# Optimization experiments

Measured on AMD Instinct MI355X. Metric: run time of the kernel, lower is better.

## Reference

```python
import jax, jax.numpy as jnp
import numpy as np

B, N, DIM = 1, 100_000, 512
HEADS, DIM_HEAD, M = 8, 64, 64


def setup_inputs() -> dict:
    key = jax.random.key(0)
    ks = jax.random.split(key, 9)
    s = 0.04  # ~ kaiming-ish scale for dim=512
    return {
        "x": jax.random.normal(ks[0], (B, N, DIM), dtype=jnp.float32),
        "temperature": jnp.full((1, HEADS, 1, 1), 0.5, dtype=jnp.float32),
        "w_slice": jax.random.normal(ks[1], (HEADS * M, DIM), dtype=jnp.float32) * s,
        "b_slice": jnp.zeros((HEADS * M,), dtype=jnp.float32),
        "w1": jax.random.normal(ks[2], (DIM_HEAD, DIM), dtype=jnp.float32) * s,
        "b1": jnp.zeros((DIM_HEAD,), dtype=jnp.float32),
        "wq": jax.random.normal(ks[3], (DIM_HEAD, DIM_HEAD), dtype=jnp.float32) * 0.125,
        "wk": jax.random.normal(ks[4], (DIM_HEAD, DIM_HEAD), dtype=jnp.float32) * 0.125,
        "wv": jax.random.normal(ks[5], (DIM_HEAD, DIM_HEAD), dtype=jnp.float32) * 0.125,
        "w3": jax.random.normal(ks[6], (DIM_HEAD, DIM_HEAD), dtype=jnp.float32) * 0.125,
        "b3": jnp.zeros((DIM_HEAD,), dtype=jnp.float32),
    }


def reference(x, temperature, w_slice, b_slice, w1, b1, wq, wk, wv, w3, b3):
    b, n, c = x.shape
    # slice logits: (B,N,H*M) -> (B,H,N,M)
    logits = jnp.einsum("bnc,ec->bne", x, w_slice) + b_slice
    logits = logits.reshape(b, n, HEADS, M).transpose(0, 2, 1, 3)
    temp = jnp.clip(temperature, 0.1, 5.0)
    w = jax.nn.softmax(logits / temp, axis=-1)          # (B,H,N,M)
    d = w.sum(axis=2)                                    # (B,H,M)
    # N -> M aggregation (w^T @ x per head)
    s_raw = jnp.einsum("bhnm,bnc->bhmc", w, x)          # (B,H,M,C)
    s = jnp.einsum("bhmc,dc->bhmd", s_raw / (d[..., None] + 1e-5), w1) + b1  # (B,H,M,dh)
    q = jnp.einsum("bhmd,ed->bhme", s, wq)
    k = jnp.einsum("bhmd,ed->bhme", s, wk)
    v = jnp.einsum("bhmd,ed->bhme", s, wv)
    scale = 1.0 / jnp.sqrt(jnp.asarray(DIM_HEAD, dtype=s.dtype))
    attn = jax.nn.softmax(jnp.einsum("bhme,bhle->bhml", q, k) * scale, axis=-1)
    s_att = jnp.einsum("bhml,bhle->bhme", attn, v)      # (B,H,M,dh)
    s_out = jnp.einsum("bhme,de->bhmd", s_att, w3) + b3
    # deslice: w @ s_out -> (B,H,N,dh) -> (B,N,H*dh)
    x_out = jnp.einsum("bhnm,bhmd->bhnd", w, s_out)
    return x_out.transpose(0, 2, 1, 3).reshape(b, n, HEADS * DIM_HEAD)
```

## Files before the change

### kernel.cpp

```cpp
#include <hip/hip_runtime.h>

typedef _Float16 f16;
typedef _Float16 f16x8 __attribute__((ext_vector_type(8)));
typedef _Float16 f16x4 __attribute__((ext_vector_type(4)));
typedef float    f32x4 __attribute__((ext_vector_type(4)));

#define N_TOK   100000
#define NPAD    100032
#define NT1     1563
#define CDIM    512
#define KSTEPS  (NPAD/32)
#define K2SPL   128

#define O_WT     ((size_t)0)
#define SZ_WT    ((size_t)512*NPAD*2)
#define O_YT     (O_WT + SZ_WT)
#define SZ_YT    ((size_t)64*NPAD*2)
#define O_WFR    (O_YT + SZ_YT)
#define SZ_WFR   ((size_t)16*4*9*64*8*2)
#define O_SPP    (O_WFR + SZ_WFR)
#define SZ_SPP   ((size_t)K2SPL*32768*4)
#define O_DPP    (O_SPP + SZ_SPP)
#define SZ_DPP   ((size_t)K2SPL*512*4)
#define O_SPRE   (O_DPP + SZ_DPP)
#define SZ_SPRE  ((size_t)32768*4)
#define O_DSTD   (O_SPRE + SZ_SPRE)
#define SZ_DSTD  ((size_t)512*4)
#define O_SOUT   (O_DSTD + SZ_DSTD)
#define SZ_SOUT  ((size_t)8*64*64*2)

__global__ void k0_pack(const float* __restrict__ wsf, const float* __restrict__ w1f,
                        f16* __restrict__ wfr) {
    int c = blockIdx.x * 256 + threadIdx.x;
    int lane = c & 63, g = c >> 6;
    int u  = g % 9,  r = g / 9;
    int we = r & 3,  kg = r >> 2;
    int col = lane & 15, quad = lane >> 4;
    int k = kg * 32 + quad * 8;
    const float* src;
    if (u < 8) src = wsf + (size_t)(we*128 + u*16 + col) * CDIM + k;
    else       src = w1f + (size_t)(we*16  + col) * CDIM + k;
    float4 a = *(const float4*)(src);
    float4 b = *(const float4*)(src + 4);
    f16x8 h;
    h[0]=(f16)a.x; h[1]=(f16)a.y; h[2]=(f16)a.z; h[3]=(f16)a.w;
    h[4]=(f16)b.x; h[5]=(f16)b.y; h[6]=(f16)b.z; h[7]=(f16)b.w;
    *(f16x8*)(wfr + (size_t)c * 8) = h;
}

#define XROW 40
#define TPITCH 72
__launch_bounds__(256, 3)
__global__ void k1_slice(const float* __restrict__ x, const float* __restrict__ temperature,
                         const f16* __restrict__ wfr, const float* __restrict__ bsl,
                         f16* __restrict__ wTf, f16* __restrict__ yTf) {
    __shared__ f16 smem[320 * TPITCH];
    f16* lX = smem;
    f16* lT = smem;
    f16* lY = smem + 256 * TPITCH;

    const int tid  = threadIdx.x;
    const int wave = tid >> 6;
    const int lane = tid & 63;
    const int quad = lane >> 4;
    const int col  = lane & 15;
    const int hgrp = blockIdx.x & 1;
    const int nt   = blockIdx.x >> 1;
    const int n0   = nt * 64;
    const int h    = hgrp * 4 + wave;

    const int srow = tid >> 2, sch = tid & 3;
    int snr = n0 + srow; if (snr > N_TOK - 1) snr = N_TOK - 1;
    const float* sbase = x + (size_t)snr * CDIM + sch * 8;

    const f16* wbase  = wfr + ((size_t)(h >> 1) * 9 + (size_t)(h & 1) * 4) * 512 + (size_t)lane * 8;
    const f16* wybase = wfr + ((size_t)wave * 9 + 8) * 512 + (size_t)lane * 8;
    const size_t KGSTR = (size_t)4 * 9 * 512;

    {
        float4 a = *(const float4*)(sbase);
        float4 bb = *(const float4*)(sbase + 4);
        f16x8 hh;
        hh[0]=(f16)a.x; hh[1]=(f16)a.y; hh[2]=(f16)a.z; hh[3]=(f16)a.w;
        hh[4]=(f16)bb.x; hh[5]=(f16)bb.y; hh[6]=(f16)bb.z; hh[7]=(f16)bb.w;
        *(f16x8*)(&lX[srow * XROW + sch * 8]) = hh;
    }

    f32x4 acc[4][5];
    #pragma unroll
    for (int nf = 0; nf < 4; ++nf)
        #pragma unroll
        for (int u = 0; u < 5; ++u) acc[nf][u] = f32x4{0.f,0.f,0.f,0.f};

    f16x8 bf[4];
    #pragma unroll
    for (int j = 0; j < 4; ++j) bf[j] = *(const f16x8*)(wbase + j * 512);
    f16x8 bfy;
    if (hgrp == 0) bfy = *(const f16x8*)(wybase);

    __syncthreads();

    #pragma unroll 2
    for (int kg = 0; kg < 16; ++kg) {
        float4 xa, xb;
        if (kg < 15) {
            xa = *(const float4*)(sbase + (kg + 1) * 32);
            xb = *(const float4*)(sbase + (kg + 1) * 32 + 4);
        }

        const f16* xbuf = lX + (kg & 1) * (64 * XROW);
        f16x8 af[4];
        #pragma unroll
        for (int nf = 0; nf < 4; ++nf)
            af[nf] = *(const f16x8*)(xbuf + (nf*16 + col) * XROW + quad * 8);

        #pragma unroll
        for (int nf = 0; nf < 4; ++nf)
            #pragma unroll
            for (int j = 0; j < 4; ++j)
                acc[nf][j] = __builtin_amdgcn_mfma_f32_16x16x32_f16(af[nf], bf[j], acc[nf][j], 0, 0, 0);
        if (hgrp == 0) {
            #pragma unroll
            for (int nf = 0; nf < 4; ++nf)
                acc[nf][4] = __builtin_amdgcn_mfma_f32_16x16x32_f16(af[nf], bfy, acc[nf][4], 0, 0, 0);
        }

        if (kg < 15) {
            const f16* wb = wbase + (size_t)(kg + 1) * KGSTR;
            #pragma unroll
            for (int j = 0; j < 4; ++j) bf[j] = *(const f16x8*)(wb + j * 512);
            if (hgrp == 0) bfy = *(const f16x8*)(wybase + (size_t)(kg + 1) * KGSTR);
        }

        if (kg < 15) {
            f16x8 hh;
            hh[0]=(f16)xa.x; hh[1]=(f16)xa.y; hh[2]=(f16)xa.z; hh[3]=(f16)xa.w;
            hh[4]=(f16)xb.x; hh[5]=(f16)xb.y; hh[6]=(f16)xb.z; hh[7]=(f16)xb.w;
            *(f16x8*)(&lX[((kg + 1) & 1) * (64 * XROW) + srow * XROW + sch * 8]) = hh;
        }
        __syncthreads();
    }

    #pragma unroll
    for (int j = 0; j < 4; ++j) {
        float bb = bsl[h*64 + j*16 + col];
        #pragma unroll
        for (int nf = 0; nf < 4; ++nf)
            #pragma unroll
            for (int r = 0; r < 4; ++r) acc[nf][j][r] += bb;
    }
    float tv = temperature[h];
    tv = fminf(fmaxf(tv, 0.1f), 5.0f);
    const float invt = 1.0f / tv;

    #pragma unroll
    for (int nf = 0; nf < 4; ++nf) {
        const int nloc = nf*16 + quad*4;
        float mx[4];
        #pragma unroll
        for (int r = 0; r < 4; ++r) {
            float m01 = fmaxf(acc[nf][0][r], acc[nf][1][r]);
            float m23 = fmaxf(acc[nf][2][r], acc[nf][3][r]);
            mx[r] = fmaxf(m01, m23);
        }
        #pragma unroll
        for (int d = 1; d < 16; d <<= 1)
            #pragma unroll
            for (int r = 0; r < 4; ++r) mx[r] = fmaxf(mx[r], __shfl_xor(mx[r], d));
        float sm[4] = {0.f, 0.f, 0.f, 0.f};
        #pragma unroll
        for (int j = 0; j < 4; ++j)
            #pragma unroll
            for (int r = 0; r < 4; ++r) {
                float ev = __expf((acc[nf][j][r] - mx[r]) * invt);
                acc[nf][j][r] = ev;
                sm[r] += ev;
            }
        #pragma unroll
        for (int d = 1; d < 16; d <<= 1)
            #pragma unroll
            for (int r = 0; r < 4; ++r) sm[r] += __shfl_xor(sm[r], d);
        #pragma unroll
        for (int r = 0; r < 4; ++r) sm[r] = 1.0f / sm[r];
        #pragma unroll
        for (int j = 0; j < 4; ++j) {
            f16x4 pk;
            #pragma unroll
            for (int r = 0; r < 4; ++r) {
                int n = n0 + nloc + r;
                float wv = (n < N_TOK) ? acc[nf][j][r] * sm[r] : 0.0f;
                pk[r] = (f16)wv;
            }
            int e_loc = wave*64 + j*16 + col;
            *(f16x4*)(lT + (size_t)e_loc*TPITCH + nloc) = pk;
        }
        if (hgrp == 0) {
            f16x4 pk;
            #pragma unroll
            for (int r = 0; r < 4; ++r) {
                int n = n0 + nloc + r;
                pk[r] = (n < N_TOK) ? (f16)acc[nf][4][r] : (f16)0.f;
            }
            *(f16x4*)(lY + (size_t)(wave*16 + col)*TPITCH + nloc) = pk;
        }
    }
    __syncthreads();

    #pragma unroll
    for (int i = 0; i < 8; ++i) {
        int gid = tid + i*256;
        int laneL = gid & 63, chunk = gid >> 6;
        int ks_loc = chunk >> 4, floc = chunk & 15;
        f16x8 v = *(const f16x8*)(lT + (size_t)(floc*16 + (laneL & 15))*TPITCH
                                     + ks_loc*32 + (laneL >> 4)*8);
        *(f16x8*)(wTf + ((size_t)((nt*2 + ks_loc)*32 + hgrp*16 + floc))*512
                       + (size_t)laneL*8) = v;
    }
    if (hgrp == 0) {
        #pragma unroll
        for (int i = 0; i < 2; ++i) {
            int gid = tid + i*256;
            int laneL = gid & 63, chunk = gid >> 6;
            int ks_loc = chunk >> 2, v4 = chunk & 3;
            f16x8 vv = *(const f16x8*)(lY + (size_t)(v4*16 + (laneL & 15))*TPITCH
                                          + ks_loc*32 + (laneL >> 4)*8);
            *(f16x8*)(yTf + ((size_t)((nt*2 + ks_loc)*4 + v4))*512
                           + (size_t)laneL*8) = vv;
        }
    }
}

#define K2_LOAD(AF, BF, kss)                                                         \
    {   _Pragma("unroll")                                                            \
        for (int v = 0; v < 4; ++v)                                                  \
            BF[v] = *(const f16x8*)(yTf + ((size_t)((kss)*4 + v))*512 + (size_t)lane*8); \
        _Pragma("unroll")                                                            \
        for (int u = 0; u < 2; ++u)                                                  \
            AF[u] = *(const f16x8*)(wTf + ((size_t)((kss)*32 + fbase + u))*512 + (size_t)lane*8); \
    }
#define K2_MFMA(AF, BF)                                                              \
    {   _Pragma("unroll")                                                            \
        for (int u = 0; u < 2; ++u) {                                                \
            _Pragma("unroll")                                                        \
            for (int v = 0; v < 4; ++v)                                              \
                acc[u][v] = __builtin_amdgcn_mfma_f32_16x16x32_f16(AF[u], BF[v], acc[u][v], 0, 0, 0); \
            float s_ = 0.f;                                                          \
            _Pragma("unroll")                                                        \
            for (int j = 0; j < 8; ++j) s_ += (float)AF[u][j];                       \
            dac[u] += s_;                                                            \
        }                                                                            \
    }
__launch_bounds__(256, 4)
__global__ void k2_spre(const f16* __restrict__ wTf, const f16* __restrict__ yTf,
                        float* __restrict__ spp, float* __restrict__ dpp) {
    const int tid = threadIdx.x, wave = tid >> 6, lane = tid & 63;
    const int quad = lane >> 4, col = lane & 15;
    const int slot = blockIdx.x >> 2, equad = blockIdx.x & 3;
    const int ebase = equad * 128 + wave * 32;
    const int fbase = equad * 8 + wave * 2;

    const int ks0 = (slot * KSTEPS) >> 7;
    const int ks1 = ((slot + 1) * KSTEPS) >> 7;

    f32x4 acc[2][4];
    float dac[2];
    #pragma unroll
    for (int u = 0; u < 2; ++u) {
        dac[u] = 0.f;
        #pragma unroll
        for (int v = 0; v < 4; ++v) acc[u][v] = f32x4{0.f,0.f,0.f,0.f};
    }

    f16x8 afA[2], bfA[4], afB[2], bfB[4];
    K2_LOAD(afA, bfA, ks0)
    int ks = ks0;
    for (; ks + 2 <= ks1; ks += 2) {
        K2_LOAD(afB, bfB, ks + 1)
        K2_MFMA(afA, bfA)
        K2_LOAD(afA, bfA, ks + 2)
        K2_MFMA(afB, bfB)
    }
    if (ks < ks1) K2_MFMA(afA, bfA)

    #pragma unroll
    for (int u = 0; u < 2; ++u) {
        dac[u] += __shfl_xor(dac[u], 16);
        dac[u] += __shfl_xor(dac[u], 32);
    }
    if (quad == 0) {
        #pragma unroll
        for (int u = 0; u < 2; ++u)
            dpp[slot*512 + ebase + u*16 + col] = dac[u];
    }
    float* dst = spp + (size_t)slot * 32768 + (size_t)equad * 8192;
    #pragma unroll
    for (int u = 0; u < 2; ++u)
        #pragma unroll
        for (int v = 0; v < 4; ++v)
            *(f32x4*)(dst + (size_t)((wave*2 + u)*4 + v)*256 + (size_t)lane*4) = acc[u][v];
}

__global__ void k2r_reduce(const float* __restrict__ spp, const float* __restrict__ dpp,
                           float* __restrict__ spre, float* __restrict__ dstd) {
    int i = blockIdx.x*256 + threadIdx.x;
    float s = 0.f;
    for (int p = 0; p < K2SPL; ++p) s += spp[(size_t)p*32768 + i];
    int r = i & 3, L = (i >> 2) & 63, v = (i >> 8) & 3, g = (i >> 10) & 7, eq = (i >> 13) & 3;
    int e = eq*128 + (g >> 1)*32 + (g & 1)*16 + (L >> 4)*4 + r;
    int d = v*16 + (L & 15);
    spre[e*64 + d] = s;
    if (i < 512) {
        float tt = 0.f;
        for (int p = 0; p < K2SPL; ++p) tt += dpp[p*512 + i];
        dstd[i] = tt;
    }
}

__global__ void k3_attn(const float* __restrict__ spre, const float* __restrict__ dstd,
                        const float* __restrict__ b1, const float* __restrict__ wq,
                        const float* __restrict__ wk, const float* __restrict__ wv,
                        const float* __restrict__ w3, const float* __restrict__ b3,
                        f16* __restrict__ sout) {
    __shared__ float wa[64][65], wb[64][65], wc[64][65];
    __shared__ float ss[64][65], kk[64][65], vv[64][65];
    __shared__ float qq[8][65], sc[8][65];
    const int h = blockIdx.x >> 3, ms = blockIdx.x & 7, tid = threadIdx.x;

    for (int i = tid; i < 4096; i += 256) {
        int r = i >> 6, c = i & 63;
        wa[r][c] = wq[i];
        wb[r][c] = wk[i];
        wc[r][c] = wv[i];
        ss[r][c] = spre[h*4096 + i] / (dstd[h*64 + r] + 1e-5f) + b1[c];
    }
    __syncthreads();

    #pragma unroll
    for (int it = 0; it < 16; ++it) {
        int m = it*4 + (tid >> 6), e = tid & 63;
        float ak = 0.f, av = 0.f;
        #pragma unroll 8
        for (int d = 0; d < 64; ++d) {
            float sv = ss[m][d];
            ak += sv * wb[e][d];
            av += sv * wc[e][d];
        }
        kk[m][e] = ak; vv[m][e] = av;
    }
    #pragma unroll
    for (int it = 0; it < 2; ++it) {
        int ml = it*4 + (tid >> 6), e = tid & 63;
        float aq = 0.f;
        #pragma unroll 8
        for (int d = 0; d < 64; ++d) aq += ss[ms*8 + ml][d] * wa[e][d];
        qq[ml][e] = aq;
    }
    __syncthreads();

    for (int i = tid; i < 4096; i += 256) wa[i >> 6][i & 63] = w3[i];
    #pragma unroll
    for (int it = 0; it < 2; ++it) {
        int ml = it*4 + (tid >> 6), l = tid & 63;
        float a = 0.f;
        #pragma unroll 8
        for (int e = 0; e < 64; ++e) a += qq[ml][e] * kk[l][e];
        sc[ml][l] = a * 0.125f;
    }
    __syncthreads();

    if (tid < 8) {
        int ml = tid;
        float mx = -1e30f;
        #pragma unroll 8
        for (int l = 0; l < 64; ++l) mx = fmaxf(mx, sc[ml][l]);
        float sm = 0.f;
        #pragma unroll 8
        for (int l = 0; l < 64; ++l) { float ev = __expf(sc[ml][l] - mx); sc[ml][l] = ev; sm += ev; }
        float rs = 1.0f / sm;
        #pragma unroll 8
        for (int l = 0; l < 64; ++l) sc[ml][l] *= rs;
    }
    __syncthreads();

    #pragma unroll
    for (int it = 0; it < 2; ++it) {
        int ml = it*4 + (tid >> 6), e = tid & 63;
        float a = 0.f;
        #pragma unroll 8
        for (int l = 0; l < 64; ++l) a += sc[ml][l] * vv[l][e];
        qq[ml][e] = a;
    }
    __syncthreads();

    #pragma unroll
    for (int it = 0; it < 2; ++it) {
        int d = it*32 + (tid >> 3), ml = tid & 7;
        float a = b3[d];
        #pragma unroll 8
        for (int e = 0; e < 64; ++e) a += qq[ml][e] * wa[d][e];
        sout[(h*64 + d)*64 + ms*8 + ml] = (f16)a;
    }
}

__launch_bounds__(256, 4)
__global__ void k4_deslice(const f16* __restrict__ wTf, const f16* __restrict__ sout,
                           float* __restrict__ out) {
    __shared__ __align__(16) char lmem[36864];
    f16*   ldsW = (f16*)lmem;
    float* ldsO = (float*)lmem;

    const int tid = threadIdx.x, wave = tid >> 6, lane = tid & 63;
    const int quad = lane >> 4, col = lane & 15;

    const int bid = blockIdx.x;
    const int xcd = bid & 7, idx = bid >> 3;
    const int q = KSTEPS >> 3, r = KSTEPS & 7;
    const int swz = (xcd < r ? xcd*(q+1) : r*(q+1) + (xcd - r)*q) + idx;
    const int n0 = swz * 32;

    const f16* srcW = wTf + (size_t)swz * 16384;
    #pragma unroll
    for (int i = 0; i < 8; ++i) {
        int id = tid + i*256;
        *(f16x8*)(ldsW + (size_t)id*8) = *(const f16x8*)(srcW + (size_t)id*8);
    }
    __syncthreads();

    f32x4 acc[2][2][4];
    #pragma unroll
    for (int hh = 0; hh < 2; ++hh)
        #pragma unroll
        for (int t = 0; t < 2; ++t)
            #pragma unroll
            for (int v = 0; v < 4; ++v) acc[hh][t][v] = f32x4{0.f,0.f,0.f,0.f};

    #pragma unroll
    for (int hh = 0; hh < 2; ++hh) {
        int h = wave*2 + hh;
        #pragma unroll
        for (int ks = 0; ks < 2; ++ks) {
            f16x8 af[2], bf[4];
            #pragma unroll
            for (int t = 0; t < 2; ++t) {
                const int fb = (h*4 + ks*2 + (quad >> 1))*512
                             + (t*2 + (col >> 3))*128 + (quad & 1)*64 + (col & 7);
                f16x8 a;
                #pragma unroll
                for (int j = 0; j < 8; ++j)
                    a[j] = ldsW[fb + j*8];
                af[t] = a;
            }
            #pragma unroll
            for (int v = 0; v < 4; ++v)
                bf[v] = *(const f16x8*)(sout + (size_t)(h*64 + v*16 + col)*64 + ks*32 + quad*8);
            #pragma unroll
            for (int t = 0; t < 2; ++t)
                #pragma unroll
                for (int v = 0; v < 4; ++v)
                    acc[hh][t][v] = __builtin_amdgcn_mfma_f32_16x16x32_f16(af[t], bf[v], acc[hh][t][v], 0, 0, 0);
        }
    }

    #pragma unroll
    for (int p = 0; p < 2; ++p) {
        __syncthreads();
        #pragma unroll
        for (int hh = 0; hh < 2; ++hh) {
            int h = wave*2 + hh;
            #pragma unroll
            for (int v = 0; v < 4; ++v)
                #pragma unroll
                for (int r2 = 0; r2 < 4; ++r2)
                    ldsO[(size_t)(quad*4 + r2)*516 + h*64 + v*16 + col] = acc[hh][p][v][r2];
        }
        __syncthreads();
        #pragma unroll
        for (int it = 0; it < 8; ++it) {
            int id = tid + it*256;
            int row = id >> 7, ch = id & 127;
            int n = n0 + p*16 + row;
            if (n < N_TOK) {
                float4 v4 = *(const float4*)(ldsO + (size_t)row*516 + ch*4);
                *(float4*)(out + (size_t)n*512 + ch*4) = v4;
            }
        }
    }
}

extern "C" void kernel_launch(void* const* d_in, const int* in_sizes, int n_in,
                              void* d_out, int out_size, void* d_ws, size_t ws_size,
                              hipStream_t stream) {
    const float* x           = (const float*)d_in[0];
    const float* temperature = (const float*)d_in[1];
    const float* w_slice     = (const float*)d_in[2];
    const float* b_slice     = (const float*)d_in[3];
    const float* w1          = (const float*)d_in[4];
    const float* b1          = (const float*)d_in[5];
    const float* wq          = (const float*)d_in[6];
    const float* wk          = (const float*)d_in[7];
    const float* wv          = (const float*)d_in[8];
    const float* w3          = (const float*)d_in[9];
    const float* b3          = (const float*)d_in[10];
    float* out = (float*)d_out;
    char*  ws  = (char*)d_ws;

    f16*   wTf   = (f16*)(ws + O_WT);
    f16*   yTf   = (f16*)(ws + O_YT);
    f16*   wfr   = (f16*)(ws + O_WFR);
    float* spp   = (float*)(ws + O_SPP);
    float* dpp   = (float*)(ws + O_DPP);
    float* spre  = (float*)(ws + O_SPRE);
    float* dstd  = (float*)(ws + O_DSTD);
    f16*   sout  = (f16*)(ws + O_SOUT);

    k0_pack<<<144, 256, 0, stream>>>(w_slice, w1, wfr);
    k1_slice<<<NT1*2, 256, 0, stream>>>(x, temperature, wfr, b_slice, wTf, yTf);
    k2_spre<<<K2SPL*4, 256, 0, stream>>>(wTf, yTf, spp, dpp);
    k2r_reduce<<<128, 256, 0, stream>>>(spp, dpp, spre, dstd);
    k3_attn<<<64, 256, 0, stream>>>(spre, dstd, b1, wq, wk, wv, w3, b3, sout);
    k4_deslice<<<KSTEPS, 256, 0, stream>>>(wTf, sout, out);
}
```

Baseline: 544.0 us.

## Manually double-buffer k1 loop, double k2 split count, use nontemporal output stores

The first kernel's K loop is unrolled by two with explicit ping-pong register sets for the weight fragments and fixed LDS buffers, so the next weight and x loads are issued before the current MFMAs. The second kernel's N-split count is doubled to 256 and its slot bounds now use a generic division, which raises parallelism but adds more partial sums to reduce. Final output stores are made nontemporal to avoid polluting cache. Together these target load latency, occupancy and write traffic, at the cost of more registers and larger reduction work.

```diff
diff --git a/kernel.cpp b/kernel.cpp
--- a/kernel.cpp
+++ b/kernel.cpp
@@ -10,7 +10,7 @@
 #define NT1     1563
 #define CDIM    512
 #define KSTEPS  (NPAD/32)
-#define K2SPL   128
+#define K2SPL   256
 
 #define O_WT     ((size_t)0)
 #define SZ_WT    ((size_t)512*NPAD*2)
@@ -92,53 +92,84 @@
         #pragma unroll
         for (int u = 0; u < 5; ++u) acc[nf][u] = f32x4{0.f,0.f,0.f,0.f};
 
-    f16x8 bf[4];
-    #pragma unroll
-    for (int j = 0; j < 4; ++j) bf[j] = *(const f16x8*)(wbase + j * 512);
-    f16x8 bfy;
-    if (hgrp == 0) bfy = *(const f16x8*)(wybase);
-
-    __syncthreads();
-
-    #pragma unroll 2
-    for (int kg = 0; kg < 16; ++kg) {
-        float4 xa, xb;
-        if (kg < 15) {
-            xa = *(const float4*)(sbase + (kg + 1) * 32);
-            xb = *(const float4*)(sbase + (kg + 1) * 32 + 4);
-        }
-
-        const f16* xbuf = lX + (kg & 1) * (64 * XROW);
-        f16x8 af[4];
-        #pragma unroll
-        for (int nf = 0; nf < 4; ++nf)
-            af[nf] = *(const f16x8*)(xbuf + (nf*16 + col) * XROW + quad * 8);
-
-        #pragma unroll
-        for (int nf = 0; nf < 4; ++nf)
-            #pragma unroll
-            for (int j = 0; j < 4; ++j)
-                acc[nf][j] = __builtin_amdgcn_mfma_f32_16x16x32_f16(af[nf], bf[j], acc[nf][j], 0, 0, 0);
-        if (hgrp == 0) {
+    f16x8 bf0[4], bf1[4], bfy0, bfy1;
+    #pragma unroll
+    for (int j = 0; j < 4; ++j) bf0[j] = *(const f16x8*)(wbase + j * 512);
+    if (hgrp == 0) bfy0 = *(const f16x8*)(wybase);
+
+    __syncthreads();
+
+    #pragma unroll 1
+    for (int kgp = 0; kgp < 8; ++kgp) {
+        {
+            const int kg = kgp * 2;
+            f16x8 af[4];
             #pragma unroll
             for (int nf = 0; nf < 4; ++nf)
-                acc[nf][4] = __builtin_amdgcn_mfma_f32_16x16x32_f16(af[nf], bfy, acc[nf][4], 0, 0, 0);
-        }
-
-        if (kg < 15) {
-            const f16* wb = wbase + (size_t)(kg + 1) * KGSTR;
-            #pragma unroll
-            for (int j = 0; j < 4; ++j) bf[j] = *(const f16x8*)(wb + j * 512);
-            if (hgrp == 0) bfy = *(const f16x8*)(wybase + (size_t)(kg + 1) * KGSTR);
-        }
-
-        if (kg < 15) {
+                af[nf] = *(const f16x8*)(lX + (nf*16 + col) * XROW + quad * 8);
+
+            {
+                const f16* wb = wbase + (size_t)(kg + 1) * KGSTR;
+                #pragma unroll
+                for (int j = 0; j < 4; ++j) bf1[j] = *(const f16x8*)(wb + j * 512);
+                if (hgrp == 0) bfy1 = *(const f16x8*)(wybase + (size_t)(kg + 1) * KGSTR);
+            }
+            float4 xa = *(const float4*)(sbase + (kg + 1) * 32);
+            float4 xb = *(const float4*)(sbase + (kg + 1) * 32 + 4);
+
+            #pragma unroll
+            for (int nf = 0; nf < 4; ++nf)
+                #pragma unroll
+                for (int j = 0; j < 4; ++j)
+                    acc[nf][j] = __builtin_amdgcn_mfma_f32_16x16x32_f16(af[nf], bf0[j], acc[nf][j], 0, 0, 0);
+            if (hgrp == 0) {
+                #pragma unroll
+                for (int nf = 0; nf < 4; ++nf)
+                    acc[nf][4] = __builtin_amdgcn_mfma_f32_16x16x32_f16(af[nf], bfy0, acc[nf][4], 0, 0, 0);
+            }
+
             f16x8 hh;
             hh[0]=(f16)xa.x; hh[1]=(f16)xa.y; hh[2]=(f16)xa.z; hh[3]=(f16)xa.w;
             hh[4]=(f16)xb.x; hh[5]=(f16)xb.y; hh[6]=(f16)xb.z; hh[7]=(f16)xb.w;
-            *(f16x8*)(&lX[((kg + 1) & 1) * (64 * XROW) + srow * XROW + sch * 8]) = hh;
-        }
-        __syncthreads();
+            *(f16x8*)(&lX[64*XROW + srow * XROW + sch * 8]) = hh;
+            __syncthreads();
+        }
+        {
+            const int kg = kgp * 2 + 1;
+            f16x8 af[4];
+            #pragma unroll
+            for (int nf = 0; nf < 4; ++nf)
+                af[nf] = *(const f16x8*)(lX + 64*XROW + (nf*16 + col) * XROW + quad * 8);
+
+            float4 xa, xb;
+            if (kgp < 7) {
+                const f16* wb = wbase + (size_t)(kg + 1) * KGSTR;
+                #pragma unroll
+                for (int j = 0; j < 4; ++j) bf0[j] = *(const f16x8*)(wb + j * 512);
+                if (hgrp == 0) bfy0 = *(const f16x8*)(wybase + (size_t)(kg + 1) * KGSTR);
+                xa = *(const float4*)(sbase + (kg + 1) * 32);
+                xb = *(const float4*)(sbase + (kg + 1) * 32 + 4);
+            }
+
+            #pragma unroll
+            for (int nf = 0; nf < 4; ++nf)
+                #pragma unroll
+                for (int j = 0; j < 4; ++j)
+                    acc[nf][j] = __builtin_amdgcn_mfma_f32_16x16x32_f16(af[nf], bf1[j], acc[nf][j], 0, 0, 0);
+            if (hgrp == 0) {
+                #pragma unroll
+                for (int nf = 0; nf < 4; ++nf)
+                    acc[nf][4] = __builtin_amdgcn_mfma_f32_16x16x32_f16(af[nf], bfy1, acc[nf][4], 0, 0, 0);
+            }
+
+            if (kgp < 7) {
+                f16x8 hh;
+                hh[0]=(f16)xa.x; hh[1]=(f16)xa.y; hh[2]=(f16)xa.z; hh[3]=(f16)xa.w;
+                hh[4]=(f16)xb.x; hh[5]=(f16)xb.y; hh[6]=(f16)xb.z; hh[7]=(f16)xb.w;
+                *(f16x8*)(&lX[srow * XROW + sch * 8]) = hh;
+            }
+            __syncthreads();
+        }
     }
 
     #pragma unroll
@@ -259,8 +290,8 @@
     const int ebase = equad * 128 + wave * 32;
     const int fbase = equad * 8 + wave * 2;
 
-    const int ks0 = (slot * KSTEPS) >> 7;
-    const int ks1 = ((slot + 1) * KSTEPS) >> 7;
+    const int ks0 = (int)(((long long)slot * KSTEPS) / K2SPL);
+    const int ks1 = (int)(((long long)(slot + 1) * KSTEPS) / K2SPL);
 
     f32x4 acc[2][4];
     float dac[2];
@@ -480,8 +511,8 @@
             int row = id >> 7, ch = id & 127;
             int n = n0 + p*16 + row;
             if (n < N_TOK) {
-                float4 v4 = *(const float4*)(ldsO + (size_t)row*516 + ch*4);
-                *(float4*)(out + (size_t)n*512 + ch*4) = v4;
+                f32x4 v4 = *(const f32x4*)(ldsO + (size_t)row*516 + ch*4);
+                __builtin_nontemporal_store(v4, (f32x4*)(out + (size_t)n*512 + ch*4));
             }
         }
     }
```

Result: faster. 531.0 us (-2.4%).
